# Kernel tuning notes

Hardware: AMD Instinct MI355X
Metric: run time of the kernel (lower is better)

The kernel has to match this reference:

```python
import jax, jax.numpy as jnp
import numpy as np
from jax import lax

D_L, D_A, D_V = 300, 74, 35
Z = 256   # zl/za/zv size (LSTM hidden)
F = 128   # fl/fa/fv size
OUT = 1
T, N = 64, 4096


def _p(key, shape, scale=0.05):
    return (jax.random.normal(key, shape, dtype=jnp.float32) * scale)


def setup_inputs() -> dict:
    key = jax.random.key(0)
    ks = iter(jax.random.split(key, 64))
    inp = {"x": jax.random.normal(next(ks), (T, N, D_L + D_A + D_V), dtype=jnp.float32)}
    for m, d in (("l", D_L), ("a", D_A), ("v", D_V)):
        inp[f"W_ih_{m}"] = _p(next(ks), (4 * Z, d))
        inp[f"W_hh_{m}"] = _p(next(ks), (4 * Z, Z))
        inp[f"b_ih_{m}"] = _p(next(ks), (4 * Z,))
        inp[f"b_hh_{m}"] = _p(next(ks), (4 * Z,))
        inp[f"Wfc_{m}"] = _p(next(ks), (Z, Z))
        inp[f"bfc_{m}"] = _p(next(ks), (Z,))
        inp[f"Wh1_{m}"] = _p(next(ks), (F, Z))
        inp[f"bh1_{m}"] = _p(next(ks), (F,))
        inp[f"Wh2_{m}"] = _p(next(ks), (F, F))
        inp[f"bh2_{m}"] = _p(next(ks), (F,))
    inp["Wy"] = _p(next(ks), (OUT, 3 * F))
    inp["by"] = _p(next(ks), (OUT,))
    return inp


def _lstm_encode(x_seq, W_ih, W_hh, b_ih, b_hh, Wfc, bfc):
    # x_seq: [t, n, d]; PyTorch LSTMCell gate order: i, f, g, o
    n = x_seq.shape[1]
    h = x_seq.dtype
    gates_x = jnp.einsum('tnd,gd->tng', x_seq, W_ih) + b_ih + b_hh  # [t,n,4Z]

    def step(carry, gx):
        hx, cx = carry
        gates = gx + hx @ W_hh.T
        i, f, g, o = jnp.split(gates, 4, axis=1)
        i = jax.nn.sigmoid(i); f = jax.nn.sigmoid(f)
        g = jnp.tanh(g);       o = jax.nn.sigmoid(o)
        cx = f * cx + i * g
        hx = o * jnp.tanh(cx)
        return (hx, cx), None

    init = (jnp.zeros((n, Z), dtype=h), jnp.zeros((n, Z), dtype=h))
    (last_h, _), _ = lax.scan(step, init, gates_x)
    return last_h @ Wfc.T + bfc  # encoderLSTM.fc1


def _head(z, W1, b1, W2, b2):
    # relu(fc2(dropout(relu(fc1(z))))) with dropout p=0 (eval)
    return jax.nn.relu(jax.nn.relu(z @ W1.T + b1) @ W2.T + b2)


def reference(x,
              W_ih_l, W_hh_l, b_ih_l, b_hh_l, Wfc_l, bfc_l, Wh1_l, bh1_l, Wh2_l, bh2_l,
              W_ih_a, W_hh_a, b_ih_a, b_hh_a, Wfc_a, bfc_a, Wh1_a, bh1_a, Wh2_a, bh2_a,
              W_ih_v, W_hh_v, b_ih_v, b_hh_v, Wfc_v, bfc_v, Wh1_v, bh1_v, Wh2_v, bh2_v,
              Wy, by):
    x_l = x[:, :, :D_L]
    x_a = x[:, :, D_L:D_L + D_A]
    x_v = x[:, :, D_L + D_A:]
    zl = _lstm_encode(x_l, W_ih_l, W_hh_l, b_ih_l, b_hh_l, Wfc_l, bfc_l)
    za = _lstm_encode(x_a, W_ih_a, W_hh_a, b_ih_a, b_hh_a, Wfc_a, bfc_a)
    zv = _lstm_encode(x_v, W_ih_v, W_hh_v, b_ih_v, b_hh_v, Wfc_v, bfc_v)
    fl = _head(zl, Wh1_l, bh1_l, Wh2_l, bh2_l)
    fa = _head(za, Wh1_a, bh1_a, Wh2_a, bh2_a)
    fv = _head(zv, Wh1_v, bh1_v, Wh2_v, bh2_v)
    fs = jnp.concatenate([fl, fa, fv], axis=1)
    y_hat = fs @ Wy.T + by
    # original returns ([x_l, x_a, x_v, y_hat], mmd_loss=0.0, missing_loss=0.0)
    return x_l, x_a, x_v, y_hat


if __name__ == "__main__":
    out = reference(**setup_inputs())
    print([o.shape for o in out])
```

## Files before the change

### kernel.cpp

```cpp
#include <hip/hip_runtime.h>

typedef __attribute__((ext_vector_type(8))) short short8;
typedef __attribute__((ext_vector_type(4))) float f32x4;
typedef unsigned short ushort_t;

#define T_DIM 64
#define N_DIM 4096
#define DL 300
#define DA 74
#define DV 35
#define DTOT 409
#define ZD 256
#define FD 128
#define KP1_L 320
#define KP1_A 96
#define KP1_V 64
#define KC_L ((KP1_L + 256) / 32)
#define KC_A ((KP1_A + 256) / 32)
#define KC_V ((KP1_V + 256) / 32)

__device__ __forceinline__ ushort_t f2bf(float v) {
    unsigned u = __float_as_uint(v);
    u += 0x7fffu + ((u >> 16) & 1u);
    return (ushort_t)(u >> 16);
}

__device__ __forceinline__ float fastrcp(float x) {
#if __has_builtin(__builtin_amdgcn_rcpf)
    return __builtin_amdgcn_rcpf(x);
#else
    return 1.f / x;
#endif
}

__device__ __forceinline__ void async_lds16(const ushort_t* g, ushort_t* l) {
    __builtin_amdgcn_global_load_lds(
        (const __attribute__((address_space(1))) unsigned int*)g,
        (__attribute__((address_space(3))) unsigned int*)l, 16, 0, 0);
}

struct PrepP {
    const float* x;
    float* ol;
    float* oa;
    float* ov;
    ushort_t* xf[3];
};
__global__ __launch_bounds__(256) void prep_kernel(PrepP p) {
    __shared__ float xrow[16][420];
    const int bid = blockIdx.x;
    const int t = bid >> 8, nb = bid & 255;
    const int tid = threadIdx.x;
    const size_t rowbase = (size_t)t * N_DIM + (size_t)nb * 16;

    const float* __restrict__ src = p.x + rowbase * DTOT;
    for (int e = tid; e < 16 * DTOT; e += 256) {
        int r = e / DTOT, d = e - r * DTOT;
        xrow[r][d] = src[e];
    }
    __syncthreads();

    {
        float* __restrict__ dl = p.ol + rowbase * DL;
        for (int e = tid; e < 16 * DL; e += 256) { int r = e / DL, d = e - r * DL; dl[e] = xrow[r][d]; }
        float* __restrict__ da = p.oa + rowbase * DA;
        for (int e = tid; e < 16 * DA; e += 256) { int r = e / DA, d = e - r * DA; da[e] = xrow[r][300 + d]; }
        float* __restrict__ dv = p.ov + rowbase * DV;
        for (int e = tid; e < 16 * DV; e += 256) { int r = e / DV, d = e - r * DV; dv[e] = xrow[r][374 + d]; }
    }

    const unsigned tnb = (unsigned)t * 256u + (unsigned)nb;
    for (int q = tid; q < 960; q += 256) {
        int m, kc, l, xkc, col0, dcap;
        if (q < 640)      { m = 0; kc = q >> 6;          l = q & 63; xkc = 10; col0 = 0;   dcap = DL; }
        else if (q < 832) { int qq = q - 640; m = 1; kc = qq >> 6; l = qq & 63; xkc = 3; col0 = 300; dcap = DA; }
        else              { int qq = q - 832; m = 2; kc = qq >> 6; l = qq & 63; xkc = 2; col0 = 374; dcap = DV; }
        int n16 = l & 15;
        int kb = kc * 32 + (l >> 4) * 8;
        ushort_t tmp[8];
#pragma unroll
        for (int j = 0; j < 8; ++j) {
            int k = kb + j;
            tmp[j] = (k < dcap) ? f2bf(xrow[n16][col0 + k]) : (ushort_t)0;
        }
        ushort_t* dst = p.xf[m] + (((size_t)tnb * xkc + kc) * 64 + l) * 8;
        *reinterpret_cast<short8*>(dst) = *reinterpret_cast<short8*>(tmp);
    }
}

struct WConvP {
    const float* Wih[3];
    const float* Whh[3];
    ushort_t* wf[3];
};
__global__ __launch_bounds__(256) void wconv_kernel(WConvP p) {
    const unsigned CL = 16u * 4 * KC_L * 64;
    const unsigned CA = 16u * 4 * KC_A * 64;
    const unsigned CV = 16u * 4 * KC_V * 64;
    unsigned e = blockIdx.x * 256u + threadIdx.x;
    int m, kcm, d, kp1;
    unsigned rel;
    if (e < CL)                { m = 0; rel = e;           kcm = KC_L; d = DL; kp1 = KP1_L; }
    else if (e < CL + CA)      { m = 1; rel = e - CL;      kcm = KC_A; d = DA; kp1 = KP1_A; }
    else if (e < CL + CA + CV) { m = 2; rel = e - CL - CA; kcm = KC_V; d = DV; kp1 = KP1_V; }
    else return;
    unsigned lane = rel & 63u;
    unsigned rest = rel >> 6;
    unsigned kc = rest % (unsigned)kcm;
    unsigned zg = rest / (unsigned)kcm;
    unsigned g = zg & 3u, zs = zg >> 2;
    unsigned row = g * 256u + zs * 16u + (lane & 15u);
    unsigned kb = kc * 32u + (lane >> 4) * 8u;
    const float* __restrict__ Wih = p.Wih[m];
    const float* __restrict__ Whh = p.Whh[m];
    ushort_t tmp[8];
#pragma unroll
    for (int j = 0; j < 8; ++j) {
        int k = (int)kb + j;
        float v = 0.f;
        if (k < d) v = Wih[(size_t)row * d + k];
        else if (k >= kp1) v = Whh[(size_t)row * 256u + (k - kp1)];
        tmp[j] = f2bf(v);
    }
    *reinterpret_cast<short8*>(p.wf[m] + (size_t)rel * 8) = *reinterpret_cast<short8*>(tmp);
}

struct ChainP {
    const ushort_t* xf[3];
    const ushort_t* wf[3];
    const float* bih[3];
    const float* bhh[3];
    float* hf;
};

template <int KP1>
__device__ __forceinline__ void chain_body(const ChainP& p, int m, int row0, ushort_t* sh) {
    constexpr int XKC = KP1 / 32;
    constexpr int KC = XKC + 8;
    constexpr int XCH = 4 * XKC;
    constexpr int XSZ = XCH * 512;
    const int tid = threadIdx.x;
    const int w = tid >> 6;
    const int lane = tid & 63, ln = lane & 15, lg = lane >> 4;
    const int nb0 = row0 >> 4;

    ushort_t* hb0 = sh;
    ushort_t* xb0 = sh + 32768;
    const ushort_t* __restrict__ xf = p.xf[m];
    const ushort_t* __restrict__ wf = p.wf[m];

    for (int e = tid; e < 8192; e += 1024) ((unsigned*)hb0)[e] = 0u;

    for (int q = w; q < XCH; q += 16) {
        int rf = q / XKC, kc = q - rf * XKC;
        const ushort_t* src = xf + (((size_t)0 * 256 + nb0 + rf) * XKC + kc) * 512 + lane * 8;
        async_lds16(src, xb0 + (size_t)q * 512);
    }

    const int z = w * 16 + ln;
    float bb4[4];
#pragma unroll
    for (int g = 0; g < 4; ++g)
        bb4[g] = p.bih[m][g * 256 + z] + p.bhh[m][g * 256 + z];
    float creg[4][4] = {};
    asm volatile("s_waitcnt vmcnt(0)" ::: "memory");
    __syncthreads();

    const int kc2 = z >> 5;
    const int bofs = ((z >> 3) & 3) * 16;
    const int jj = z & 7;
    const ushort_t* __restrict__ wfz = wf + (size_t)w * 4 * KC * 512;

#pragma unroll 1
    for (int t = 0; t < T_DIM; ++t) {
        const ushort_t* __restrict__ xbc = xb0 + (size_t)(t & 1) * XSZ;
        const ushort_t* __restrict__ hbc = hb0 + (size_t)(t & 1) * 16384;
        ushort_t* __restrict__ hbn = hb0 + (size_t)((t & 1) ^ 1) * 16384;

        f32x4 acc[4][4] = {};
#pragma unroll 1
        for (int kc = 0; kc < KC; ++kc) {
            short8 b[4];
#pragma unroll
            for (int g = 0; g < 4; ++g)
                b[g] = *reinterpret_cast<const short8*>(
                    wfz + ((size_t)g * KC + kc) * 512 + lane * 8);
            short8 a[4];
            if (kc < XKC) {
#pragma unroll
                for (int rf = 0; rf < 4; ++rf)
                    a[rf] = *reinterpret_cast<const short8*>(
                        xbc + ((size_t)(rf * XKC + kc) * 64 + lane) * 8);
            } else {
#pragma unroll
                for (int rf = 0; rf < 4; ++rf)
                    a[rf] = *reinterpret_cast<const short8*>(
                        hbc + ((size_t)(rf * 8 + (kc - XKC)) * 64 + lane) * 8);
            }
#pragma unroll
            for (int g = 0; g < 4; ++g)
#pragma unroll
                for (int rf = 0; rf < 4; ++rf)
                    acc[rf][g] = __builtin_amdgcn_mfma_f32_16x16x32_bf16(
                        a[rf], b[g], acc[rf][g], 0, 0, 0);
        }

        if (t + 1 < T_DIM) {
            ushort_t* xbn = xb0 + (size_t)((t & 1) ^ 1) * XSZ;
            for (int q = w; q < XCH; q += 16) {
                int rf = q / XKC, kc = q - rf * XKC;
                const ushort_t* src =
                    xf + (((size_t)(t + 1) * 256 + nb0 + rf) * XKC + kc) * 512 + lane * 8;
                async_lds16(src, xbn + (size_t)q * 512);
            }
        }

#pragma unroll
        for (int rf = 0; rf < 4; ++rf) {
#pragma unroll
            for (int reg = 0; reg < 4; ++reg) {
                float gi = acc[rf][0][reg] + bb4[0];
                float gf = acc[rf][1][reg] + bb4[1];
                float gg = acc[rf][2][reg] + bb4[2];
                float go = acc[rf][3][reg] + bb4[3];
                float i_ = fastrcp(1.f + __expf(-gi));
                float f_ = fastrcp(1.f + __expf(-gf));
                float g_ = 1.f - 2.f * fastrcp(1.f + __expf(2.f * gg));
                float o_ = fastrcp(1.f + __expf(-go));
                float cc = f_ * creg[rf][reg] + i_ * g_;
                creg[rf][reg] = cc;
                float hh = o_ * (1.f - 2.f * fastrcp(1.f + __expf(2.f * cc)));
                hbn[((size_t)(rf * 8 + kc2) * 64 + (lg * 4 + reg + bofs)) * 8 + jj] = f2bf(hh);
                if (t == T_DIM - 1) {
                    int nl = rf * 16 + lg * 4 + reg;
                    p.hf[(size_t)m * N_DIM * ZD + (size_t)(row0 + nl) * ZD + z] = hh;
                }
            }
        }

        asm volatile("s_waitcnt vmcnt(0)" ::: "memory");
        __syncthreads();
    }
}

__global__ __launch_bounds__(1024)
__attribute__((amdgpu_waves_per_eu(4, 4)))
void lstm_chain_kernel(ChainP p) {
    __shared__ ushort_t sh[73728];
    const int bid = blockIdx.x;
    const int r8 = bid & 7, idx = bid >> 3;
    const int m = idx >> 3;
    const int bm = (idx & 7) * 8 + r8;
    const int row0 = bm * 64;
    if (m == 0)      chain_body<KP1_L>(p, 0, row0, sh);
    else if (m == 1) chain_body<KP1_A>(p, 1, row0, sh);
    else             chain_body<KP1_V>(p, 2, row0, sh);
}

struct GemmP {
    const float* A1[3];
    const float* W1[3];
    const float* b1[3];
    float* C[3];
    int K1[3];
    int lda1;
    int ldc;
    int relu;
};

__device__ __forceinline__ void mac16(const float (&As)[16][64], const float (&Ws)[16][64],
                                      int tx, int ty, float (&acc)[4][4]) {
#pragma unroll
    for (int k = 0; k < 16; ++k) {
        float4 av = *reinterpret_cast<const float4*>(&As[k][ty * 4]);
        float4 bv = *reinterpret_cast<const float4*>(&Ws[k][tx * 4]);
        float a[4] = {av.x, av.y, av.z, av.w};
        float b[4] = {bv.x, bv.y, bv.z, bv.w};
#pragma unroll
        for (int i = 0; i < 4; ++i)
#pragma unroll
            for (int j = 0; j < 4; ++j)
                acc[i][j] = fmaf(a[i], b[j], acc[i][j]);
    }
}

__global__ __launch_bounds__(256) void gemm3_kernel(GemmP p) {
    const int m = blockIdx.z;
    const float* __restrict__ A1 = p.A1[m];
    const float* __restrict__ W1 = p.W1[m];
    const int K1 = p.K1[m];
    float* __restrict__ C = p.C[m];
    const int row0 = blockIdx.x * 64;
    const int col0 = blockIdx.y * 64;

    __shared__ __align__(16) float As[16][64];
    __shared__ __align__(16) float Ws[16][64];

    const int tid = threadIdx.x;
    const int tx = tid & 15, ty = tid >> 4;
    float acc[4][4] = {};

    for (int k0 = 0; k0 < K1; k0 += 16) {
#pragma unroll
        for (int i = 0; i < 4; ++i) {
            int e = tid * 4 + i;
            int rr = e >> 4, k = e & 15;
            int kk = k0 + k;
            As[k][rr] = (kk < K1) ? A1[(size_t)(row0 + rr) * p.lda1 + kk] : 0.f;
            Ws[k][rr] = (kk < K1) ? W1[(size_t)(col0 + rr) * K1 + kk] : 0.f;
        }
        __syncthreads();
        mac16(As, Ws, tx, ty, acc);
        __syncthreads();
    }

    const float* __restrict__ b1 = p.b1[m];
#pragma unroll
    for (int i = 0; i < 4; ++i) {
        int rr = row0 + ty * 4 + i;
        float v[4];
#pragma unroll
        for (int j = 0; j < 4; ++j) {
            int cc = col0 + tx * 4 + j;
            float tvl = acc[i][j] + b1[cc];
            if (p.relu) tvl = fmaxf(tvl, 0.f);
            v[j] = tvl;
        }
        float4 o = make_float4(v[0], v[1], v[2], v[3]);
        *reinterpret_cast<float4*>(&C[(size_t)rr * p.ldc + col0 + tx * 4]) = o;
    }
}

__global__ __launch_bounds__(256) void y_kernel(const float* __restrict__ fs,
                                                const float* __restrict__ Wy,
                                                const float* __restrict__ by,
                                                float* __restrict__ y) {
    unsigned wave = (blockIdx.x * 256u + threadIdx.x) >> 6;
    unsigned lane = threadIdx.x & 63u;
    if (wave >= N_DIM) return;
    const float* row = fs + (size_t)wave * 3 * FD;
    float s = 0.f;
    for (unsigned j = lane; j < 3 * FD; j += 64) s += row[j] * Wy[j];
#pragma unroll
    for (int off = 32; off; off >>= 1) s += __shfl_down(s, off);
    if (lane == 0) y[wave] = s + by[0];
}

extern "C" void kernel_launch(void* const* d_in, const int* in_sizes, int n_in,
                              void* d_out, int out_size, void* d_ws, size_t ws_size,
                              hipStream_t stream) {
    const float* x = (const float*)d_in[0];
    const float *W_ih[3], *W_hh[3], *b_ih[3], *b_hh[3], *Wfc[3], *bfc[3],
                *Wh1[3], *bh1[3], *Wh2[3], *bh2[3];
    for (int m = 0; m < 3; ++m) {
        const int b = 1 + m * 10;
        W_ih[m] = (const float*)d_in[b + 0];
        W_hh[m] = (const float*)d_in[b + 1];
        b_ih[m] = (const float*)d_in[b + 2];
        b_hh[m] = (const float*)d_in[b + 3];
        Wfc[m]  = (const float*)d_in[b + 4];
        bfc[m]  = (const float*)d_in[b + 5];
        Wh1[m]  = (const float*)d_in[b + 6];
        bh1[m]  = (const float*)d_in[b + 7];
        Wh2[m]  = (const float*)d_in[b + 8];
        bh2[m]  = (const float*)d_in[b + 9];
    }
    const float* Wy = (const float*)d_in[31];
    const float* by = (const float*)d_in[32];

    float* out   = (float*)d_out;
    float* out_l = out;
    float* out_a = out_l + (size_t)T_DIM * N_DIM * DL;
    float* out_v = out_a + (size_t)T_DIM * N_DIM * DA;
    float* out_y = out_v + (size_t)T_DIM * N_DIM * DV;

    const size_t NZ = (size_t)N_DIM * ZD;
    const size_t NF = (size_t)N_DIM * FD;
    const size_t WFL = (size_t)16 * 4 * KC_L * 512;
    const size_t WFA = (size_t)16 * 4 * KC_A * 512;
    const size_t WFV = (size_t)16 * 4 * KC_V * 512;

    char* wsb = (char*)d_ws;
    float* hf   = (float*)wsb;
    float* zbuf = hf + 3 * NZ;
    float* f1   = zbuf + 3 * NZ;
    float* fs   = f1 + 3 * NF;
    ushort_t* wf_l = (ushort_t*)(fs + 3 * NF);
    ushort_t* wf_a = wf_l + WFL;
    ushort_t* wf_v = wf_a + WFA;
    ushort_t* xf_l = wf_v + WFV;
    ushort_t* xf_a = xf_l + (size_t)T_DIM * N_DIM * KP1_L;
    ushort_t* xf_v = xf_a + (size_t)T_DIM * N_DIM * KP1_A;
    size_t need = (size_t)((char*)(xf_v + (size_t)T_DIM * N_DIM * KP1_V) - wsb);
    if (ws_size < need) return;

    {
        WConvP p{};
        for (int m = 0; m < 3; ++m) { p.Wih[m] = W_ih[m]; p.Whh[m] = W_hh[m]; }
        p.wf[0] = wf_l; p.wf[1] = wf_a; p.wf[2] = wf_v;
        wconv_kernel<<<(16 * 4 * (KC_L + KC_A + KC_V) * 64) / 256, 256, 0, stream>>>(p);
    }

    {
        PrepP p{};
        p.x = x;
        p.ol = out_l; p.oa = out_a; p.ov = out_v;
        p.xf[0] = xf_l; p.xf[1] = xf_a; p.xf[2] = xf_v;
        prep_kernel<<<T_DIM * 256, 256, 0, stream>>>(p);
    }

    {
        ChainP cp{};
        cp.xf[0] = xf_l; cp.xf[1] = xf_a; cp.xf[2] = xf_v;
        cp.wf[0] = wf_l; cp.wf[1] = wf_a; cp.wf[2] = wf_v;
        for (int m = 0; m < 3; ++m) { cp.bih[m] = b_ih[m]; cp.bhh[m] = b_hh[m]; }
        cp.hf = hf;
        lstm_chain_kernel<<<192, 1024, 0, stream>>>(cp);
    }

    {
        GemmP p{};
        for (int m = 0; m < 3; ++m) {
            p.A1[m] = hf + m * NZ; p.W1[m] = Wfc[m]; p.K1[m] = ZD;
            p.b1[m] = bfc[m];      p.C[m] = zbuf + m * NZ;
        }
        p.lda1 = ZD; p.ldc = ZD; p.relu = 0;
        gemm3_kernel<<<dim3(N_DIM / 64, ZD / 64, 3), 256, 0, stream>>>(p);
    }
    {
        GemmP p{};
        for (int m = 0; m < 3; ++m) {
            p.A1[m] = zbuf + m * NZ; p.W1[m] = Wh1[m]; p.K1[m] = ZD;
            p.b1[m] = bh1[m];        p.C[m] = f1 + m * NF;
        }
        p.lda1 = ZD; p.ldc = FD; p.relu = 1;
        gemm3_kernel<<<dim3(N_DIM / 64, FD / 64, 3), 256, 0, stream>>>(p);
    }
    {
        GemmP p{};
        for (int m = 0; m < 3; ++m) {
            p.A1[m] = f1 + m * NF; p.W1[m] = Wh2[m]; p.K1[m] = FD;
            p.b1[m] = bh2[m];      p.C[m] = fs + m * FD;
        }
        p.lda1 = FD; p.ldc = 3 * FD; p.relu = 1;
        gemm3_kernel<<<dim3(N_DIM / 64, FD / 64, 3), 256, 0, stream>>>(p);
    }
    y_kernel<<<(N_DIM * 64) / 256, 256, 0, stream>>>(fs, Wy, by, out_y);
}
```

Before: 1.258 ms.

## Split language-modality LSTM across block pairs exchanging hidden halves via global flags

The language LSTM (largest input width) is now split across two cooperating blocks per 64-row tile. Each block computes half of the hidden units and swaps its half of h with its partner every timestep through global memory, using a flag spin-wait. The grid grows from 192 to 256 blocks and is launched cooperatively so all blocks are co-resident. This balances the heavier language chain against the audio and video chains. It costs a per-step cross-block handshake and global round trip, and relies on co-residency.

After: 1.860 ms. +47.8%, slower.

```diff
diff --git a/kernel.cpp b/kernel.cpp
--- a/kernel.cpp
+++ b/kernel.cpp
@@ -131,10 +131,218 @@
     const float* bih[3];
     const float* bhh[3];
     float* hf;
+    ushort_t* hx;
+    unsigned* flags;
 };
 
+__device__ void lhalf_body(const ChainP& p, int P, int zh, int bid, int partner,
+                           ushort_t* sh) {
+    constexpr int XKC = 10, KC = 18, XCH = 40, XSZ = XCH * 512;
+    const int tid = threadIdx.x;
+    const int w = tid >> 6, lane = tid & 63, ln = lane & 15, lg = lane >> 4;
+    const int zs_l = w >> 1;
+    const int rh = w & 1;
+    const int row0 = P * 64;
+    const int nb0 = row0 >> 4;
+
+    ushort_t* hb0 = sh;
+    ushort_t* xb0 = sh + 32768;
+    const ushort_t* __restrict__ xf = p.xf[0];
+    const ushort_t* __restrict__ wf = p.wf[0];
+
+    for (int e = tid; e < 8192; e += 1024) ((unsigned*)hb0)[e] = 0u;
+
+    for (int q = w; q < XCH; q += 16) {
+        int rf = q / XKC, kc = q - rf * XKC;
+        async_lds16(xf + (((size_t)0 * 256 + nb0 + rf) * XKC + kc) * 512 + lane * 8,
+                    xb0 + (size_t)q * 512);
+    }
+
+    const int z = zh * 128 + zs_l * 16 + ln;
+    float bb4[4];
+#pragma unroll
+    for (int g = 0; g < 4; ++g)
+        bb4[g] = p.bih[0][g * 256 + z] + p.bhh[0][g * 256 + z];
+    float creg[2][4] = {};
+    asm volatile("s_waitcnt vmcnt(0)" ::: "memory");
+    __syncthreads();
+
+    const int kc2own0 = 4 * zh, kc2par0 = 4 * (1 - zh);
+    const int zs_g = zh * 8 + zs_l;
+    const ushort_t* __restrict__ wfz = wf + (size_t)zs_g * 4 * KC * 512;
+    const int hkc2 = z >> 5;
+    const int bofs = ((z >> 3) & 3) * 16;
+    const int jj = z & 7;
+    unsigned* myflag = p.flags + (size_t)bid * 16;
+    const unsigned* pflag = p.flags + (size_t)partner * 16;
+
+#pragma unroll 1
+    for (int t = 0; t < T_DIM; ++t) {
+        const ushort_t* __restrict__ xbc = xb0 + (size_t)(t & 1) * XSZ;
+        ushort_t* __restrict__ hbc = hb0 + (size_t)(t & 1) * 16384;
+        ushort_t* __restrict__ hbn = hb0 + (size_t)((t & 1) ^ 1) * 16384;
+
+        f32x4 acc[2][4] = {};
+        short8 bcur[4], bnxt[4];
+
+#pragma unroll
+        for (int g = 0; g < 4; ++g)
+            bcur[g] = *reinterpret_cast<const short8*>(wfz + ((size_t)g * KC) * 512 + lane * 8);
+#pragma unroll 1
+        for (int kc = 0; kc < XKC; ++kc) {
+            if (kc + 1 < XKC) {
+#pragma unroll
+                for (int g = 0; g < 4; ++g)
+                    bnxt[g] = *reinterpret_cast<const short8*>(
+                        wfz + ((size_t)g * KC + kc + 1) * 512 + lane * 8);
+            }
+            short8 a[2];
+#pragma unroll
+            for (int rfi = 0; rfi < 2; ++rfi)
+                a[rfi] = *reinterpret_cast<const short8*>(
+                    xbc + ((size_t)((rh * 2 + rfi) * XKC + kc) * 64 + lane) * 8);
+#pragma unroll
+            for (int g = 0; g < 4; ++g)
+#pragma unroll
+                for (int rfi = 0; rfi < 2; ++rfi)
+                    acc[rfi][g] = __builtin_amdgcn_mfma_f32_16x16x32_bf16(
+                        a[rfi], bcur[g], acc[rfi][g], 0, 0, 0);
+            if (kc + 1 < XKC) {
+#pragma unroll
+                for (int g = 0; g < 4; ++g) bcur[g] = bnxt[g];
+            }
+        }
+
+#pragma unroll
+        for (int g = 0; g < 4; ++g)
+            bcur[g] = *reinterpret_cast<const short8*>(
+                wfz + ((size_t)g * KC + XKC + kc2own0) * 512 + lane * 8);
+#pragma unroll
+        for (int k2 = 0; k2 < 4; ++k2) {
+            const int kc2 = kc2own0 + k2;
+            if (k2 < 3) {
+#pragma unroll
+                for (int g = 0; g < 4; ++g)
+                    bnxt[g] = *reinterpret_cast<const short8*>(
+                        wfz + ((size_t)g * KC + XKC + kc2 + 1) * 512 + lane * 8);
+            }
+            short8 a[2];
+#pragma unroll
+            for (int rfi = 0; rfi < 2; ++rfi)
+                a[rfi] = *reinterpret_cast<const short8*>(
+                    hbc + ((size_t)((rh * 2 + rfi) * 8 + kc2) * 64 + lane) * 8);
+#pragma unroll
+            for (int g = 0; g < 4; ++g)
+#pragma unroll
+                for (int rfi = 0; rfi < 2; ++rfi)
+                    acc[rfi][g] = __builtin_amdgcn_mfma_f32_16x16x32_bf16(
+                        a[rfi], bcur[g], acc[rfi][g], 0, 0, 0);
+            if (k2 < 3) {
+#pragma unroll
+                for (int g = 0; g < 4; ++g) bcur[g] = bnxt[g];
+            }
+        }
+
+        if (t > 0) {
+            if (tid == 0) {
+                while (__hip_atomic_load(pflag, __ATOMIC_RELAXED, __HIP_MEMORY_SCOPE_AGENT)
+                       < (unsigned)t)
+                    __builtin_amdgcn_s_sleep(1);
+            }
+            __syncthreads();
+            {
+                const int rf = w >> 2, k2l = w & 3;
+                const int kc2 = kc2par0 + k2l;
+                const ushort_t* src = p.hx +
+                    ((((size_t)(t & 1) * 64 + P) * 2 + (1 - zh)) * 16 + w) * 512 + lane * 8;
+                short8 v = *(const volatile short8*)src;
+                *reinterpret_cast<short8*>(hbc + ((size_t)(rf * 8 + kc2) * 64 + lane) * 8) = v;
+            }
+            __syncthreads();
+        }
+
+#pragma unroll
+        for (int g = 0; g < 4; ++g)
+            bcur[g] = *reinterpret_cast<const short8*>(
+                wfz + ((size_t)g * KC + XKC + kc2par0) * 512 + lane * 8);
+#pragma unroll
+        for (int k2 = 0; k2 < 4; ++k2) {
+            const int kc2 = kc2par0 + k2;
+            if (k2 < 3) {
+#pragma unroll
+                for (int g = 0; g < 4; ++g)
+                    bnxt[g] = *reinterpret_cast<const short8*>(
+                        wfz + ((size_t)g * KC + XKC + kc2 + 1) * 512 + lane * 8);
+            }
+            short8 a[2];
+#pragma unroll
+            for (int rfi = 0; rfi < 2; ++rfi)
+                a[rfi] = *reinterpret_cast<const short8*>(
+                    hbc + ((size_t)((rh * 2 + rfi) * 8 + kc2) * 64 + lane) * 8);
+#pragma unroll
+            for (int g = 0; g < 4; ++g)
+#pragma unroll
+                for (int rfi = 0; rfi < 2; ++rfi)
+                    acc[rfi][g] = __builtin_amdgcn_mfma_f32_16x16x32_bf16(
+                        a[rfi], bcur[g], acc[rfi][g], 0, 0, 0);
+            if (k2 < 3) {
+#pragma unroll
+                for (int g = 0; g < 4; ++g) bcur[g] = bnxt[g];
+            }
+        }
+
+        if (t + 1 < T_DIM) {
+            ushort_t* xbn = xb0 + (size_t)((t & 1) ^ 1) * XSZ;
+            for (int q = w; q < XCH; q += 16) {
+                int rf = q / XKC, kc = q - rf * XKC;
+                async_lds16(xf + (((size_t)(t + 1) * 256 + nb0 + rf) * XKC + kc) * 512 + lane * 8,
+                            xbn + (size_t)q * 512);
+            }
+        }
+
+#pragma unroll
+        for (int rfi = 0; rfi < 2; ++rfi) {
+            const int rf = rh * 2 + rfi;
+#pragma unroll
+            for (int reg = 0; reg < 4; ++reg) {
+                float gi = acc[rfi][0][reg] + bb4[0];
+                float gf = acc[rfi][1][reg] + bb4[1];
+                float gg = acc[rfi][2][reg] + bb4[2];
+                float go = acc[rfi][3][reg] + bb4[3];
+                float i_ = fastrcp(1.f + __expf(-gi));
+                float f_ = fastrcp(1.f + __expf(-gf));
+                float g_ = 1.f - 2.f * fastrcp(1.f + __expf(2.f * gg));
+                float o_ = fastrcp(1.f + __expf(-go));
+                float cc = f_ * creg[rfi][reg] + i_ * g_;
+                creg[rfi][reg] = cc;
+                float hh = o_ * (1.f - 2.f * fastrcp(1.f + __expf(2.f * cc)));
+                hbn[((size_t)(rf * 8 + hkc2) * 64 + (lg * 4 + reg + bofs)) * 8 + jj] = f2bf(hh);
+                if (t == T_DIM - 1) {
+                    int nl = rf * 16 + lg * 4 + reg;
+                    p.hf[(size_t)(row0 + nl) * ZD + z] = hh;
+                }
+            }
+        }
+        __syncthreads();
+
+        if (t + 1 < T_DIM) {
+            const int rf = w >> 2, k2l = w & 3;
+            const int kc2 = kc2own0 + k2l;
+            short8 v = *reinterpret_cast<const short8*>(
+                hbn + ((size_t)(rf * 8 + kc2) * 64 + lane) * 8);
+            *(volatile short8*)(p.hx +
+                ((((size_t)((t + 1) & 1) * 64 + P) * 2 + zh) * 16 + w) * 512 + lane * 8) = v;
+        }
+        asm volatile("s_waitcnt vmcnt(0)" ::: "memory");
+        if (tid == 0 && t + 1 < T_DIM)
+            __hip_atomic_store(myflag, (unsigned)(t + 1),
+                               __ATOMIC_RELAXED, __HIP_MEMORY_SCOPE_AGENT);
+        __syncthreads();
+    }
+}
+
 template <int KP1>
-__device__ __forceinline__ void chain_body(const ChainP& p, int m, int row0, ushort_t* sh) {
+__device__ void av_body(const ChainP& p, int m, int row0, ushort_t* sh) {
     constexpr int XKC = KP1 / 32;
     constexpr int KC = XKC + 8;
     constexpr int XCH = 4 * XKC;
@@ -153,8 +361,8 @@
 
     for (int q = w; q < XCH; q += 16) {
         int rf = q / XKC, kc = q - rf * XKC;
-        const ushort_t* src = xf + (((size_t)0 * 256 + nb0 + rf) * XKC + kc) * 512 + lane * 8;
-        async_lds16(src, xb0 + (size_t)q * 512);
+        async_lds16(xf + (((size_t)0 * 256 + nb0 + rf) * XKC + kc) * 512 + lane * 8,
+                    xb0 + (size_t)q * 512);
     }
 
     const int z = w * 16 + ln;
@@ -209,9 +417,8 @@
             ushort_t* xbn = xb0 + (size_t)((t & 1) ^ 1) * XSZ;
             for (int q = w; q < XCH; q += 16) {
                 int rf = q / XKC, kc = q - rf * XKC;
-                const ushort_t* src =
-                    xf + (((size_t)(t + 1) * 256 + nb0 + rf) * XKC + kc) * 512 + lane * 8;
-                async_lds16(src, xbn + (size_t)q * 512);
+                async_lds16(xf + (((size_t)(t + 1) * 256 + nb0 + rf) * XKC + kc) * 512 + lane * 8,
+                            xbn + (size_t)q * 512);
             }
         }
 
@@ -249,12 +456,15 @@
     __shared__ ushort_t sh[73728];
     const int bid = blockIdx.x;
     const int r8 = bid & 7, idx = bid >> 3;
-    const int m = idx >> 3;
-    const int bm = (idx & 7) * 8 + r8;
-    const int row0 = bm * 64;
-    if (m == 0)      chain_body<KP1_L>(p, 0, row0, sh);
-    else if (m == 1) chain_body<KP1_A>(p, 1, row0, sh);
-    else             chain_body<KP1_V>(p, 2, row0, sh);
+    if (idx < 16) {
+        const int P = (idx >> 1) * 8 + r8;
+        const int zh = idx & 1;
+        lhalf_body(p, P, zh, bid, bid ^ 8, sh);
+    } else if (idx < 24) {
+        av_body<KP1_A>(p, 1, ((idx - 16) * 8 + r8) * 64, sh);
+    } else {
+        av_body<KP1_V>(p, 2, ((idx - 24) * 8 + r8) * 64, sh);
+    }
 }
 
 struct GemmP {
@@ -379,13 +589,16 @@
     const size_t WFL = (size_t)16 * 4 * KC_L * 512;
     const size_t WFA = (size_t)16 * 4 * KC_A * 512;
     const size_t WFV = (size_t)16 * 4 * KC_V * 512;
+    const size_t HX  = (size_t)2 * 64 * 2 * 16 * 512;
 
     char* wsb = (char*)d_ws;
-    float* hf   = (float*)wsb;
+    unsigned* flags = (unsigned*)wsb;
+    float* hf   = (float*)(wsb + 16384);
     float* zbuf = hf + 3 * NZ;
     float* f1   = zbuf + 3 * NZ;
     float* fs   = f1 + 3 * NF;
-    ushort_t* wf_l = (ushort_t*)(fs + 3 * NF);
+    ushort_t* hx   = (ushort_t*)(fs + 3 * NF);
+    ushort_t* wf_l = hx + HX;
     ushort_t* wf_a = wf_l + WFL;
     ushort_t* wf_v = wf_a + WFA;
     ushort_t* xf_l = wf_v + WFV;
@@ -394,6 +607,8 @@
     size_t need = (size_t)((char*)(xf_v + (size_t)T_DIM * N_DIM * KP1_V) - wsb);
     if (ws_size < need) return;
 
+    hipMemsetAsync(wsb, 0, 16384, stream);
+
     {
         WConvP p{};
         for (int m = 0; m < 3; ++m) { p.Wih[m] = W_ih[m]; p.Whh[m] = W_hh[m]; }
@@ -414,8 +629,13 @@
         cp.xf[0] = xf_l; cp.xf[1] = xf_a; cp.xf[2] = xf_v;
         cp.wf[0] = wf_l; cp.wf[1] = wf_a; cp.wf[2] = wf_v;
         for (int m = 0; m < 3; ++m) { cp.bih[m] = b_ih[m]; cp.bhh[m] = b_hh[m]; }
-        cp.hf = hf;
-        lstm_chain_kernel<<<192, 1024, 0, stream>>>(cp);
+        cp.hf = hf; cp.hx = hx; cp.flags = flags;
+        void* args[] = {&cp};
+        hipError_t ce = hipLaunchCooperativeKernel((void*)lstm_chain_kernel,
+                                                   dim3(256), dim3(1024), args, 0, stream);
+        if (ce != hipSuccess) {
+            lstm_chain_kernel<<<256, 1024, 0, stream>>>(cp);
+        }
     }
 
     {
```
